# Performance work log

Hardware: AMD Instinct MI355X
Metric: run time of the kernel (lower is better)

Reference implementation:

```python
import jax, jax.numpy as jnp
import numpy as np

B, C, H, W = 16, 64, 64, 64  # z_e shape; C == embedding_dim
K = 1024                     # num_embeddings
COMMITMENT_COST = 0.25
EPS = 1e-5


def setup_inputs() -> dict:
    key = jax.random.key(0)
    k1, k2 = jax.random.split(key)
    z_e = jax.random.normal(k1, (B, C, H, W), dtype=jnp.float32)
    # codebook init ~ U(-1/D, 1/D) as in the torch module
    emb_w = jax.random.uniform(k2, (K, C), dtype=jnp.float32, minval=-1.0 / C, maxval=1.0 / C)
    return {"z_e": z_e, "emb_w": emb_w}


def reference(z_e, emb_w):
    orig_dtype = z_e.dtype
    b, c, h, w = z_e.shape
    z = z_e.astype(jnp.float32)
    # per-channel std over (batch, h, w); computed under no_grad in torch -> stop_gradient
    std = jax.lax.stop_gradient(
        jnp.clip(jnp.std(z, axis=(0, 2, 3), keepdims=True, ddof=1), EPS, None)
    )
    z = z / std                                        # [b,c,h,w]
    zf = z.transpose(0, 2, 3, 1).reshape(-1, c)        # [N, c]
    ew = emb_w.astype(jnp.float32)                     # [K, c]
    # squared euclidean distances: ||z||^2 - 2 z.e + ||e||^2  -> [N, K]
    d = (
        jnp.sum(zf * zf, axis=1, keepdims=True)
        - 2.0 * (zf @ ew.T)
        + jnp.sum(ew * ew, axis=1)
    )
    idx = jnp.argmin(d, axis=1)                        # [N]
    z_q = ew[idx].reshape(b, h, w, c).transpose(0, 3, 1, 2)  # [b,c,h,w]
    z_sg = jax.lax.stop_gradient(z)
    commitment = COMMITMENT_COST * jnp.mean((z_sg - z_q) ** 2)
    codebook = jnp.mean((z_sg - z_q) ** 2)             # eval-mode codebook loss
    vq_loss = commitment + codebook
    z_q_st = (z + jax.lax.stop_gradient(z_q - z)).astype(orig_dtype)
    n_tokens = idx.shape[0]
    counts = jnp.zeros((K,), dtype=jnp.float32).at[idx].add(1.0)
    avg_probs = counts / n_tokens
    perplexity = jnp.exp(-jnp.sum(avg_probs * jnp.log(jnp.clip(avg_probs, 1e-10, None))))
    indices = idx.reshape(b, h, w)
    return z_q_st, vq_loss, perplexity, indices
```

## Files before the change

kernel.cpp:

```cpp
#include <hip/hip_runtime.h>
#include <math.h>
#include <float.h>

#define HW 4096
#define CHW 262144
#define NTOK 65536
#define NELEM 4194304

#define WS_LOSS 0
#define WS_PART 1024
#define WS_EE   2048
#define WS_E2   3072
#define WS_HIST 68608
#define WS_DONE 69632

#define EPSM 2.0e-4f

typedef __attribute__((ext_vector_type(8))) short bf16x8;
typedef __attribute__((ext_vector_type(4))) float f32x4;

__device__ __forceinline__ unsigned short f2bf(float x) {
  unsigned u = __float_as_uint(x);
  u += 0x7FFFu + ((u >> 16) & 1u);
  return (unsigned short)(u >> 16);
}
__device__ __forceinline__ float bf2f(unsigned short h) {
  return __uint_as_float(((unsigned)h) << 16);
}
__device__ __forceinline__ void gload_lds16(const unsigned short* g, unsigned short* l) {
  __builtin_amdgcn_global_load_lds(
      (const __attribute__((address_space(1))) unsigned int*)g,
      (__attribute__((address_space(3))) unsigned int*)l, 16, 0, 0);
}

__global__ __launch_bounds__(1024) void k_pre(const float* __restrict__ z,
                                              const float* __restrict__ emb,
                                              double* __restrict__ part,
                                              unsigned short* __restrict__ e2g,
                                              float* __restrict__ eeg,
                                              int* __restrict__ hist,
                                              int* __restrict__ done) {
  __shared__ double rs[16], rs2[16];
  int tid = threadIdx.x;
  int blk = blockIdx.x;
  if (blk == 0 && tid == 0) *done = 0;
  if (blk < 256) {
    int c = blk & 63, q = blk >> 6;
    double s = 0.0, s2 = 0.0;
    const float* base = z + (size_t)c * HW;
    #pragma unroll
    for (int jj = 0; jj < 4; ++jj) {
      int bb = (q << 2) + jj;
      float4 v = *(const float4*)(base + (size_t)bb * CHW + (tid << 2));
      s  += (double)v.x + (double)v.y + (double)v.z + (double)v.w;
      s2 += (double)v.x * v.x + (double)v.y * v.y + (double)v.z * v.z + (double)v.w * v.w;
    }
    for (int o = 32; o > 0; o >>= 1) {
      s += __shfl_down(s, o, 64);
      s2 += __shfl_down(s2, o, 64);
    }
    int wv = tid >> 6, ln = tid & 63;
    if (ln == 0) { rs[wv] = s; rs2[wv] = s2; }
    __syncthreads();
    if (tid == 0) {
      double S = 0.0, S2 = 0.0;
      #pragma unroll
      for (int w = 0; w < 16; ++w) { S += rs[w]; S2 += rs2[w]; }
      part[(c << 2) + q] = S;
      part[256 + (c << 2) + q] = S2;
    }
  } else {
    int ct = blk - 256;
    if (ct == 0) hist[tid] = 0;
    int k0 = ct << 6;
    int code = tid >> 4, c4 = tid & 15;
    float4 v = *(const float4*)(emb + (size_t)((k0 + code) << 6) + (c4 << 2));
    unsigned short h0 = f2bf(v.x), h1 = f2bf(v.y), h2 = f2bf(v.z), h3 = f2bf(v.w);
    unsigned short l0 = f2bf(v.x - bf2f(h0)), l1 = f2bf(v.y - bf2f(h1));
    unsigned short l2 = f2bf(v.z - bf2f(h2)), l3 = f2bf(v.w - bf2f(h3));
    int jL = (c4 >> 1) & 3;
    int e = (c4 & 1) << 2;
    int cH = code >> 4, cL = code & 15;
    size_t base = (size_t)ct * 8192 + cH * 512 + jL * 128 + cL * 8 + e;
    int jHh = c4 >> 3;
    *(uint2*)(e2g + base + (size_t)jHh * 2048) =
        make_uint2((unsigned)h0 | ((unsigned)h1 << 16), (unsigned)h2 | ((unsigned)h3 << 16));
    *(uint2*)(e2g + base + (size_t)(2 + jHh) * 2048) =
        make_uint2((unsigned)l0 | ((unsigned)l1 << 16), (unsigned)l2 | ((unsigned)l3 << 16));
    if (tid < 64) {
      const float* er = emb + (size_t)((k0 + tid) << 6);
      float s = 0.f;
      #pragma unroll
      for (int c = 0; c < 64; ++c) s = fmaf(er[c], er[c], s);
      eeg[k0 + tid] = s;
    }
  }
}

__global__ __launch_bounds__(256, 2) void k_vq(
    const float* __restrict__ z_e, const float* __restrict__ emb,
    const double* __restrict__ part, const float* __restrict__ eeg,
    const unsigned short* __restrict__ e2g,
    float* __restrict__ out_zq, float* __restrict__ out_idx,
    float* __restrict__ loss_part, int* __restrict__ done,
    float* __restrict__ out_scalars, int* __restrict__ hist) {
  __shared__ unsigned short A2[8192];
  __shared__ unsigned short B2[8192];
  __shared__ float sEE[1024];
  __shared__ float sRstd[64];
  __shared__ double rl[4], rh[4];
  __shared__ int lastFlag;
  float* hs1 = (float*)A2;
  float* hs2 = (float*)A2 + 256;
  float* hs3 = (float*)A2 + 512;
  int*   hk1 = (int*)A2 + 768;
  int*   hk2 = (int*)A2 + 1024;
  int*   skf = (int*)A2 + 1280;
  int*   mk2f = (int*)A2 + 1344;
  int*   pairL = (int*)A2 + 1408;
  int*   fullL = (int*)A2 + 1472;
  int*   cntB = (int*)A2 + 1536;
  int*   cntC = (int*)A2 + 1537;
  float* sred = (float*)A2 + 1540;
  float* zf   = (float*)A2 + 1544;
  float* fbd4 = (float*)A2 + 1608;
  int*   fbk4 = (int*)A2 + 1612;

  int tid = threadIdx.x;
  int lane = tid & 63;
  int wv = tid >> 6;
  int blk = blockIdx.x;
  int b = blk >> 6;
  int s0 = (blk & 63) << 6;

  {
    float4 ev = ((const float4*)eeg)[tid];
    ev.x += 8.0f; ev.y += 8.0f; ev.z += 8.0f; ev.w += 8.0f;
    ((float4*)sEE)[tid] = ev;
  }

  if (tid < 64) {
    double S = 0.0, S2 = 0.0;
    #pragma unroll
    for (int q = 0; q < 4; ++q) {
      S += part[(tid << 2) + q];
      S2 += part[256 + (tid << 2) + q];
    }
    const double N = (double)NTOK;
    double var = (S2 - S * S / N) / (N - 1.0);
    float sd = fmaxf((float)sqrt(var), 1e-5f);
    sRstd[tid] = 1.0f / sd;
  }
  __syncthreads();

  {
    int t = tid & 63, q = tid >> 6;
    int half = q >> 1, jl0 = (q & 1) << 1;
    const float* zsrc = z_e + (size_t)b * CHW + (size_t)(q << 4) * HW + s0 + t;
    unsigned hw_[8], lw_[8];
    #pragma unroll
    for (int cc = 0; cc < 16; ++cc) {
      float v = zsrc[(size_t)cc * HW] * sRstd[(q << 4) + cc];
      unsigned short h = f2bf(v);
      unsigned short l = f2bf(v - bf2f(h));
      if (cc & 1) { hw_[cc >> 1] |= ((unsigned)h) << 16; lw_[cc >> 1] |= ((unsigned)l) << 16; }
      else        { hw_[cc >> 1] = h;                    lw_[cc >> 1] = l; }
    }
    int base = (t >> 4) * 512 + (t & 15) * 8;
    #pragma unroll
    for (int u = 0; u < 2; ++u) {
      *(uint4*)(A2 + half * 2048 + base + (jl0 + u) * 128) =
          make_uint4(hw_[4 * u], hw_[4 * u + 1], hw_[4 * u + 2], hw_[4 * u + 3]);
      *(uint4*)(A2 + (2 + half) * 2048 + base + (jl0 + u) * 128) =
          make_uint4(lw_[4 * u], lw_[4 * u + 1], lw_[4 * u + 2], lw_[4 * u + 3]);
    }
  }

  int quad = lane >> 4, l15 = lane & 15;

  {
    const unsigned short* gsrc = e2g + wv * 512 + (lane << 3);
    unsigned short* ldst = B2 + wv * 512;
    #pragma unroll
    for (int rr = 0; rr < 4; ++rr)
      gload_lds16(gsrc + rr * 2048, ldst + rr * 2048);
  }
  __syncthreads();

  bf16x8 afc[4][4];
  #pragma unroll
  for (int j = 0; j < 4; ++j)
    #pragma unroll
    for (int mt = 0; mt < 4; ++mt)
      afc[j][mt] = *(const bf16x8*)(A2 + j * 2048 + mt * 512 + quad * 128 + l15 * 8);
  __syncthreads();

  float ts1[16], ts2[16], ts3[16];
  #pragma unroll
  for (int i = 0; i < 16; ++i) { ts1[i] = FLT_MAX; ts2[i] = FLT_MAX; ts3[i] = FLT_MAX; }

  const int aJH[6] = {0, 1, 2, 3, 0, 1};
  const int bJH[6] = {0, 1, 0, 1, 2, 3};

  #pragma unroll 1
  for (int ct = 0; ct < 16; ++ct) {
    const unsigned short* bb = (ct & 1) ? A2 : B2;
    if (ct < 15) {
      const unsigned short* gsrc = e2g + (size_t)(ct + 1) * 8192 + wv * 512 + (lane << 3);
      unsigned short* ldst = (((ct + 1) & 1) ? A2 : B2) + wv * 512;
      #pragma unroll
      for (int rr = 0; rr < 4; ++rr)
        gload_lds16(gsrc + rr * 2048, ldst + rr * 2048);
    }
    float ee0 = sEE[(ct << 6) + (wv << 4) + l15];

    f32x4 acc[4];
    #pragma unroll
    for (int mt = 0; mt < 4; ++mt) acc[mt] = (f32x4)(0.f);

    #pragma unroll
    for (int s = 0; s < 6; ++s) {
      bf16x8 bfr = *(const bf16x8*)(bb + bJH[s] * 2048 + wv * 512 + quad * 128 + l15 * 8);
      #pragma unroll
      for (int mt = 0; mt < 4; ++mt)
        acc[mt] = __builtin_amdgcn_mfma_f32_16x16x32_bf16(afc[aJH[s]][mt], bfr, acc[mt], 0, 0, 0);
    }

    unsigned ctu = (unsigned)ct;
    #pragma unroll
    for (int mt = 0; mt < 4; ++mt) {
      #pragma unroll
      for (int r = 0; r < 4; ++r) {
        float sv = fmaf(-2.0f, acc[mt][r], ee0);
        sv = fmaxf(sv, 0.25f);
        float p = __uint_as_float((__float_as_uint(sv) & 0xFFFFFFF0u) | ctu);
        int sl = (mt << 2) + r;
        float t1o = ts1[sl], t2o = ts2[sl];
        ts1[sl] = fminf(p, t1o);
        ts2[sl] = fminf(fmaxf(p, t1o), t2o);
        ts3[sl] = fminf(fmaxf(p, t2o), ts3[sl]);
      }
    }
    if (ct < 15) __syncthreads();
  }
  __syncthreads();

  int tk1[16], tk2[16];
  #pragma unroll
  for (int sl = 0; sl < 16; ++sl) {
    unsigned b1 = __float_as_uint(ts1[sl]);
    unsigned b2 = __float_as_uint(ts2[sl]);
    tk1[sl] = (int)(((b1 & 15u) << 6) | ((unsigned)wv << 4) | (unsigned)l15);
    tk2[sl] = (int)(((b2 & 15u) << 6) | ((unsigned)wv << 4) | (unsigned)l15);
    ts1[sl] = __uint_as_float(b1 & ~15u);
    ts2[sl] = __uint_as_float(b2 & ~15u);
    ts3[sl] = __uint_as_float(__float_as_uint(ts3[sl]) & ~15u);
  }

  #pragma unroll
  for (int m = 1; m <= 8; m <<= 1) {
    #pragma unroll
    for (int sl = 0; sl < 16; ++sl) {
      float ob1 = __shfl_xor(ts1[sl], m, 64); int oq1 = __shfl_xor(tk1[sl], m, 64);
      float ob2 = __shfl_xor(ts2[sl], m, 64); int oq2 = __shfl_xor(tk2[sl], m, 64);
      float ob3 = __shfl_xor(ts3[sl], m, 64);
      bool t1 = (ts1[sl] < ob1) || (ts1[sl] == ob1 && tk1[sl] < oq1);
      float o1 = t1 ? ts1[sl] : ob1; int ok1 = t1 ? tk1[sl] : oq1;
      float aH = t1 ? ts2[sl] : ts1[sl]; int aHk = t1 ? tk2[sl] : tk1[sl]; float aH2 = t1 ? ts3[sl] : ts2[sl];
      float bH = t1 ? ob1 : ob2;         int bHk = t1 ? oq1 : oq2;         float bH2 = t1 ? ob2 : ob3;
      bool t2 = (aH < bH) || (aH == bH && aHk < bHk);
      float o2 = t2 ? aH : bH; int ok2 = t2 ? aHk : bHk;
      float aI = t2 ? aH2 : aH;
      float bI = t2 ? bH : bH2;
      ts1[sl] = o1; tk1[sl] = ok1; ts2[sl] = o2; tk2[sl] = ok2; ts3[sl] = fminf(aI, bI);
    }
  }
  if (tid == 0) { *cntB = 0; *cntC = 0; }
  if (l15 == 0) {
    #pragma unroll
    for (int mt = 0; mt < 4; ++mt)
      #pragma unroll
      for (int r = 0; r < 4; ++r) {
        int t = (mt << 4) + (quad << 2) + r;
        int sl = (mt << 2) + r;
        hs1[(wv << 6) + t] = ts1[sl]; hs2[(wv << 6) + t] = ts2[sl]; hs3[(wv << 6) + t] = ts3[sl];
        hk1[(wv << 6) + t] = tk1[sl]; hk2[(wv << 6) + t] = tk2[sl];
      }
  }
  __syncthreads();

  if (tid < 64) {
    float a1 = hs1[tid], a2 = hs2[tid], a3 = hs3[tid];
    int e1 = hk1[tid], e2v = hk2[tid];
    #pragma unroll
    for (int w = 1; w < 4; ++w) {
      float b1 = hs1[(w << 6) + tid], b2 = hs2[(w << 6) + tid], b3 = hs3[(w << 6) + tid];
      int f1 = hk1[(w << 6) + tid], f2 = hk2[(w << 6) + tid];
      bool t1 = (a1 < b1) || (a1 == b1 && e1 < f1);
      float o1 = t1 ? a1 : b1; int ok1 = t1 ? e1 : f1;
      float aH = t1 ? a2 : a1; int aHk = t1 ? e2v : e1; float aH2 = t1 ? a3 : a2;
      float bH = t1 ? b1 : b2; int bHk = t1 ? f1 : f2; float bH2 = t1 ? b2 : b3;
      bool t2 = (aH < bH) || (aH == bH && aHk < bHk);
      a1 = o1; e1 = ok1;
      a2 = t2 ? aH : bH; e2v = t2 ? aHk : bHk;
      a3 = fminf(t2 ? aH2 : aH, t2 ? bH : bH2);
    }
    skf[tid] = e1;
    mk2f[tid] = e2v;
    if (a2 - a1 <= EPSM) {
      if (a3 - a1 > EPSM) { int p = atomicAdd(cntB, 1); pairL[p] = tid; }
      else                { int p = atomicAdd(cntC, 1); fullL[p] = tid; }
    }
  }
  __syncthreads();

  int nB = *cntB, nC = *cntC;

  if (tid < nB) {
    int t = pairL[tid];
    int ka = skf[t], kb = mk2f[t];
    const float* za = z_e + (size_t)b * CHW + s0 + t;
    const float* ea = emb + ((size_t)ka << 6);
    const float* ebp = emb + ((size_t)kb << 6);
    float zz = 0.f, da = 0.f, db = 0.f;
    #pragma unroll
    for (int c = 0; c < 64; ++c) {
      float zv = za[(size_t)c * HW] * sRstd[c];
      zz = fmaf(zv, zv, zz);
      da = fmaf(ea[c], zv, da);
      db = fmaf(ebp[c], zv, db);
    }
    float d1 = (zz - 2.0f * da) + eeg[ka];
    float d2 = (zz - 2.0f * db) + eeg[kb];
    if (d2 < d1 || (d2 == d1 && kb < ka)) skf[t] = kb;
  }
  __syncthreads();

  for (int i = 0; i < nC; ++i) {
    int t = fullL[i];
    if (tid < 64) zf[tid] = z_e[(size_t)b * CHW + (size_t)tid * HW + s0 + t] * sRstd[tid];
    __syncthreads();
    const float4* zf4 = (const float4*)zf;
    const float* er0 = emb + ((size_t)(tid << 2) << 6);
    float zz = 0.f;
    float dot[4] = {0.f, 0.f, 0.f, 0.f};
    #pragma unroll
    for (int c4 = 0; c4 < 16; ++c4) {
      float4 zv = zf4[c4];
      zz = fmaf(zv.x, zv.x, zz); zz = fmaf(zv.y, zv.y, zz);
      zz = fmaf(zv.z, zv.z, zz); zz = fmaf(zv.w, zv.w, zz);
      #pragma unroll
      for (int j = 0; j < 4; ++j) {
        float4 ev = *(const float4*)(er0 + (j << 6) + (c4 << 2));
        dot[j] = fmaf(ev.x, zv.x, dot[j]);
        dot[j] = fmaf(ev.y, zv.y, dot[j]);
        dot[j] = fmaf(ev.z, zv.z, dot[j]);
        dot[j] = fmaf(ev.w, zv.w, dot[j]);
      }
    }
    float bdl = FLT_MAX; int bkl = 0;
    #pragma unroll
    for (int j = 0; j < 4; ++j) {
      float dd = (zz - 2.0f * dot[j]) + eeg[(tid << 2) + j];
      if (dd < bdl) { bdl = dd; bkl = (tid << 2) + j; }
    }
    #pragma unroll
    for (int m = 1; m <= 32; m <<= 1) {
      float od = __shfl_xor(bdl, m, 64);
      int   ok = __shfl_xor(bkl, m, 64);
      if (od < bdl || (od == bdl && ok < bkl)) { bdl = od; bkl = ok; }
    }
    if (lane == 0) { fbd4[wv] = bdl; fbk4[wv] = bkl; }
    __syncthreads();
    if (tid == 0) {
      float bb2 = fbd4[0]; int kk2 = fbk4[0];
      #pragma unroll
      for (int w = 1; w < 4; ++w)
        if (fbd4[w] < bb2 || (fbd4[w] == bb2 && fbk4[w] < kk2)) { bb2 = fbd4[w]; kk2 = fbk4[w]; }
      skf[t] = kk2;
    }
    __syncthreads();
  }
  __syncthreads();

  if (tid < 64) {
    int k = skf[tid];
    out_idx[(blk << 6) + tid] = (float)k;
    atomicAdd(&hist[k], 1);
  }

  {
    int t = tid & 63;
    int g = tid >> 6;
    int kq = skf[t];
    const float* eq = emb + ((size_t)kq << 6) + (g << 4);
    const float* zb2 = z_e + (size_t)b * CHW + (size_t)(g << 4) * HW + s0 + t;
    float* ob = out_zq + (size_t)b * CHW + (size_t)(g << 4) * HW + s0 + t;
    float lsum = 0.f;
    #pragma unroll
    for (int j4 = 0; j4 < 4; ++j4) {
      float4 ev = *(const float4*)(eq + (j4 << 2));
      #pragma unroll
      for (int u = 0; u < 4; ++u) {
        int jj = (j4 << 2) + u;
        float zv = zb2[(size_t)jj * HW] * sRstd[(g << 4) + jj];
        float e = (&ev.x)[u];
        float df = zv - e;
        lsum = fmaf(df, df, lsum);
        ob[(size_t)jj * HW] = zv + (e - zv);
      }
    }
    for (int o = 32; o > 0; o >>= 1) lsum += __shfl_down(lsum, o, 64);
    if (lane == 0) sred[wv] = lsum;
  }
  __syncthreads();

  if (tid == 0) {
    loss_part[blk] = sred[0] + sred[1] + sred[2] + sred[3];
    __threadfence();
    int prev = atomicAdd(done, 1);
    lastFlag = (prev == 1023);
  }
  __syncthreads();
  if (!lastFlag) return;

  double ls = (double)loss_part[tid] + (double)loss_part[tid + 256]
            + (double)loss_part[tid + 512] + (double)loss_part[tid + 768];
  double hsum = 0.0;
  #pragma unroll
  for (int jj = 0; jj < 4; ++jj) {
    float p = (float)hist[tid + (jj << 8)] * (1.0f / 65536.0f);
    float lg = logf(fmaxf(p, 1e-10f));
    hsum += (double)(p * lg);
  }
  for (int o = 32; o > 0; o >>= 1) {
    ls += __shfl_down(ls, o, 64);
    hsum += __shfl_down(hsum, o, 64);
  }
  if (lane == 0) { rl[wv] = ls; rh[wv] = hsum; }
  __syncthreads();
  if (tid == 0) {
    double L = rl[0] + rl[1] + rl[2] + rl[3];
    double Hn = rh[0] + rh[1] + rh[2] + rh[3];
    float m = (float)(L / (double)NELEM);
    out_scalars[0] = 0.25f * m + m;
    out_scalars[1] = expf((float)(-Hn));
  }
}

extern "C" void kernel_launch(void* const* d_in, const int* in_sizes, int n_in,
                              void* d_out, int out_size, void* d_ws, size_t ws_size,
                              hipStream_t stream) {
  const float* z_e = (const float*)d_in[0];
  const float* emb = (const float*)d_in[1];
  float* ws = (float*)d_ws;
  float* loss_part = ws + WS_LOSS;
  double* part = (double*)(ws + WS_PART);
  float* eeg = ws + WS_EE;
  unsigned short* e2g = (unsigned short*)(ws + WS_E2);
  int* hist = (int*)(ws + WS_HIST);
  int* done = (int*)(ws + WS_DONE);

  float* out = (float*)d_out;
  float* out_zq = out;
  float* out_scalars = out + NELEM;
  float* out_idx = out + NELEM + 2;

  k_pre<<<272, 1024, 0, stream>>>(z_e, emb, part, e2g, eeg, hist, done);
  k_vq<<<1024, 256, 0, stream>>>(z_e, emb, part, eeg, e2g, out_zq, out_idx,
                                 loss_part, done, out_scalars, hist);
}
```

Before: 193.0 us.

## Triple-buffer codebook prefetch with vmcnt waits and nontemporal z_e/output accesses

```diff
diff --git a/kernel.cpp b/kernel.cpp
--- a/kernel.cpp
+++ b/kernel.cpp
@@ -105,7 +105,9 @@
     float* __restrict__ loss_part, int* __restrict__ done,
     float* __restrict__ out_scalars, int* __restrict__ hist) {
   __shared__ unsigned short A2[8192];
-  __shared__ unsigned short B2[8192];
+  __shared__ unsigned short Bb0[8192];
+  __shared__ unsigned short Bb1[8192];
+  __shared__ unsigned short Bb2[8192];
   __shared__ float sEE[1024];
   __shared__ float sRstd[64];
   __shared__ double rl[4], rh[4];
@@ -133,6 +135,16 @@
   int b = blk >> 6;
   int s0 = (blk & 63) << 6;
 
+  const unsigned short* gbase = e2g + wv * 512 + (lane << 3);
+  {
+    unsigned short* d0 = Bb0 + wv * 512;
+    unsigned short* d1 = Bb1 + wv * 512;
+    #pragma unroll
+    for (int rr = 0; rr < 4; ++rr) gload_lds16(gbase + rr * 2048, d0 + rr * 2048);
+    #pragma unroll
+    for (int rr = 0; rr < 4; ++rr) gload_lds16(gbase + 8192 + rr * 2048, d1 + rr * 2048);
+  }
+
   {
     float4 ev = ((const float4*)eeg)[tid];
     ev.x += 8.0f; ev.y += 8.0f; ev.z += 8.0f; ev.w += 8.0f;
@@ -160,7 +172,8 @@
     unsigned hw_[8], lw_[8];
     #pragma unroll
     for (int cc = 0; cc < 16; ++cc) {
-      float v = zsrc[(size_t)cc * HW] * sRstd[(q << 4) + cc];
+      float zraw = __builtin_nontemporal_load(zsrc + (size_t)cc * HW);
+      float v = zraw * sRstd[(q << 4) + cc];
       unsigned short h = f2bf(v);
       unsigned short l = f2bf(v - bf2f(h));
       if (cc & 1) { hw_[cc >> 1] |= ((unsigned)h) << 16; lw_[cc >> 1] |= ((unsigned)l) << 16; }
@@ -175,17 +188,9 @@
           make_uint4(lw_[4 * u], lw_[4 * u + 1], lw_[4 * u + 2], lw_[4 * u + 3]);
     }
   }
+  __syncthreads();
 
   int quad = lane >> 4, l15 = lane & 15;
-
-  {
-    const unsigned short* gsrc = e2g + wv * 512 + (lane << 3);
-    unsigned short* ldst = B2 + wv * 512;
-    #pragma unroll
-    for (int rr = 0; rr < 4; ++rr)
-      gload_lds16(gsrc + rr * 2048, ldst + rr * 2048);
-  }
-  __syncthreads();
 
   bf16x8 afc[4][4];
   #pragma unroll
@@ -193,7 +198,6 @@
     #pragma unroll
     for (int mt = 0; mt < 4; ++mt)
       afc[j][mt] = *(const bf16x8*)(A2 + j * 2048 + mt * 512 + quad * 128 + l15 * 8);
-  __syncthreads();
 
   float ts1[16], ts2[16], ts3[16];
   #pragma unroll
@@ -204,13 +208,17 @@
 
   #pragma unroll 1
   for (int ct = 0; ct < 16; ++ct) {
-    const unsigned short* bb = (ct & 1) ? A2 : B2;
-    if (ct < 15) {
-      const unsigned short* gsrc = e2g + (size_t)(ct + 1) * 8192 + wv * 512 + (lane << 3);
-      unsigned short* ldst = (((ct + 1) & 1) ? A2 : B2) + wv * 512;
+    int r = ct % 3;
+    const unsigned short* bb = (r == 0) ? Bb0 : (r == 1) ? Bb1 : Bb2;
+    if (ct < 15) asm volatile("s_waitcnt vmcnt(4)" ::: "memory");
+    else         asm volatile("s_waitcnt vmcnt(0)" ::: "memory");
+    if (ct <= 13) {
+      int rw = (ct + 2) % 3;
+      unsigned short* wd = ((rw == 0) ? Bb0 : (rw == 1) ? Bb1 : Bb2) + wv * 512;
+      const unsigned short* gs = e2g + (size_t)(ct + 2) * 8192 + wv * 512 + (lane << 3);
       #pragma unroll
       for (int rr = 0; rr < 4; ++rr)
-        gload_lds16(gsrc + rr * 2048, ldst + rr * 2048);
+        gload_lds16(gs + rr * 2048, wd + rr * 2048);
     }
     float ee0 = sEE[(ct << 6) + (wv << 4) + l15];
 
@@ -230,18 +238,17 @@
     #pragma unroll
     for (int mt = 0; mt < 4; ++mt) {
       #pragma unroll
-      for (int r = 0; r < 4; ++r) {
-        float sv = fmaf(-2.0f, acc[mt][r], ee0);
+      for (int r2 = 0; r2 < 4; ++r2) {
+        float sv = fmaf(-2.0f, acc[mt][r2], ee0);
         sv = fmaxf(sv, 0.25f);
         float p = __uint_as_float((__float_as_uint(sv) & 0xFFFFFFF0u) | ctu);
-        int sl = (mt << 2) + r;
+        int sl = (mt << 2) + r2;
         float t1o = ts1[sl], t2o = ts2[sl];
         ts1[sl] = fminf(p, t1o);
         ts2[sl] = fminf(fmaxf(p, t1o), t2o);
         ts3[sl] = fminf(fmaxf(p, t2o), ts3[sl]);
       }
     }
-    if (ct < 15) __syncthreads();
   }
   __syncthreads();
 
@@ -385,7 +392,7 @@
 
   if (tid < 64) {
     int k = skf[tid];
-    out_idx[(blk << 6) + tid] = (float)k;
+    __builtin_nontemporal_store((float)k, &out_idx[(blk << 6) + tid]);
     atomicAdd(&hist[k], 1);
   }
 
@@ -403,11 +410,12 @@
       #pragma unroll
       for (int u = 0; u < 4; ++u) {
         int jj = (j4 << 2) + u;
-        float zv = zb2[(size_t)jj * HW] * sRstd[(g << 4) + jj];
+        float zraw = __builtin_nontemporal_load(zb2 + (size_t)jj * HW);
+        float zv = zraw * sRstd[(g << 4) + jj];
         float e = (&ev.x)[u];
         float df = zv - e;
         lsum = fmaf(df, df, lsum);
-        ob[(size_t)jj * HW] = zv + (e - zv);
+        __builtin_nontemporal_store(zv + (e - zv), ob + (size_t)jj * HW);
       }
     }
     for (int o = 32; o > 0; o >>= 1) lsum += __shfl_down(lsum, o, 64);
```

Measured after the change: 200.2 us. +3.7%, slower.
